# Optimization experiments

Hardware: AMD Instinct MI355X
Metric: run time of the kernel (lower is better)

The kernel has to match this reference:

```python
import jax, jax.numpy as jnp
import numpy as np

B, C, V = 4096, 1000, 8000   # batch, NUM_COMPO, NUM_CHARS
THRESH = 0.8                 # compo_score_thresh
SCALE = 0.1                  # score_adjustment_scale
TOPK = 5


def setup_inputs() -> dict:
    key = jax.random.key(0)
    k1, k2, k3, k4 = jax.random.split(key, 4)
    return {
        "pred_class_logits": jax.random.normal(k1, (B, V), jnp.float32),
        "pred_compo_logits": jax.random.normal(k2, (B, C), jnp.float32),
        "compo_co_occurrence_prob": jax.random.uniform(k3, (C, C), dtype=jnp.float32),
        "compo_chinese_matrix": jax.random.randint(k4, (C, V), 0, 2, dtype=jnp.int32),
    }


def _decode_one(compo_scores, co_occ, matrix):
    """components_to_chinese_char for one sample. compo_scores:[C], co_occ:[C,C], matrix:[C,V]."""
    nC, nV = matrix.shape
    # score adjustment from co-occurrence of components above threshold
    sel = compo_scores > THRESH                                   # [C]
    adj = SCALE * jnp.sum(
        jnp.where(sel[:, None], co_occ * compo_scores[:, None], 0.0), axis=0)  # [C]
    scores = compo_scores + adj
    max_idx = jnp.argmax(scores)
    max_score = scores[max_idx]
    # re-threshold and sort selected scores descending (fixed-shape: mask with -inf)
    sel2 = scores > THRESH
    num_selected = jnp.sum(sel2.astype(jnp.int32))
    masked = jnp.where(sel2, scores, -jnp.inf)
    order = jnp.argsort(-masked)          # descending; selected compo indices first
    sorted_scores = masked[order]
    hit0 = matrix[max_idx]                # [V] 0/1

    def cond(carry):
        i, hit, _ = carry
        return (i < num_selected) & (jnp.sum(hit) > 1)

    def body(carry):
        i, hit, _ = carry
        row = matrix[order[i]]
        new_hit = jnp.where(hit + row == 2, 1, 0).astype(jnp.int32)  # intersection
        return (i + 1, new_hit, hit)

    i0 = jnp.array(1, jnp.int32)
    i, hit, prev = jax.lax.while_loop(cond, body, (i0, hit0, hit0))
    empty = jnp.sum(hit) == 0
    i = jnp.where(empty, i - 1, i)
    hit = jnp.where(empty, prev, hit)
    hit_score = jnp.where(i == 1, max_score, sorted_scores[jnp.maximum(i - 1, 0)])
    # first 5 hit char indices (ascending, as tf.where yields), padded with -1
    char_ids = jnp.where(hit == 1, jnp.arange(nV), nV)
    first5 = jnp.sort(char_ids)[:TOPK]
    hit_indices = jnp.where(first5 == nV, -1, first5).astype(jnp.int32)
    return hit_indices, hit_score


def reference(pred_class_logits, pred_compo_logits, compo_co_occurrence_prob, compo_chinese_matrix):
    class_probs = jax.nn.softmax(pred_class_logits, axis=1)            # [B,V]
    class_scores, class_indices = jax.lax.top_k(class_probs, TOPK)     # [B,5]
    compo_scores = jax.nn.sigmoid(pred_compo_logits)                   # [B,C]
    hit_indices, hit_scores = jax.vmap(_decode_one, in_axes=(0, None, None))(
        compo_scores, compo_co_occurrence_prob, compo_chinese_matrix)
    class_indices = class_indices.astype(jnp.int32)
    num_hit = jnp.sum((hit_indices != -1).astype(jnp.int32), axis=1)   # [B]
    combined1 = jnp.where(num_hit == 1, hit_indices[:, 0], class_indices[:, 0])
    combined2 = jnp.where((class_scores[:, 0] < 0.85) & (num_hit == 1),
                          hit_indices[:, 0], class_indices[:, 0])
    return (class_indices, class_scores, hit_indices, hit_scores, combined1, combined2)
```

## Files before the change

### kernel.cpp

```cpp
#include <hip/hip_runtime.h>
#include <cstdint>
#include <cstddef>

typedef unsigned long long u64;

#define B_SZ 4096
#define C_SZ 1000
#define V_SZ 8000
#define RW 128
#define THRESHF 0.8f
#define SCALEF 0.1f

#define OFF_CI 0
#define OFF_CS (B_SZ * 5)
#define OFF_HI (2 * B_SZ * 5)
#define OFF_HS (3 * B_SZ * 5)
#define OFF_C1 (3 * B_SZ * 5 + B_SZ)
#define OFF_C2 (3 * B_SZ * 5 + 2 * B_SZ)

__global__ __launch_bounds__(256) void pack_kernel(const int* __restrict__ mat,
                                                   u64* __restrict__ packed) {
  const int c = blockIdx.x;
  const int tid = threadIdx.x;
  const int lane = tid & 63;
  const int wv = tid >> 6;
  const int* row = mat + (size_t)c * V_SZ;
  for (int base = 0; base < 8192; base += 256) {
    const int k = base + tid;
    int v = 0;
    if (k < V_SZ) v = row[k];
    u64 msk = __ballot(v != 0);
    if (lane == 0) packed[(size_t)c * RW + ((base >> 6) + wv)] = msk;
  }
}

__global__ __launch_bounds__(256) void class_topk_kernel(const float* __restrict__ logits,
                                                         float* __restrict__ out) {
  const int b = blockIdx.x;
  const int tid = threadIdx.x;
  const int lane = tid & 63;
  const int wv = tid >> 6;
  const float* row = logits + (size_t)b * V_SZ;
  float v[32];
#pragma unroll
  for (int f = 0; f < 8; ++f) {
    const int base = (f << 10) + (tid << 2);
    if (base < V_SZ) {
      float4 x = *(const float4*)(row + base);
      v[4 * f + 0] = x.x; v[4 * f + 1] = x.y; v[4 * f + 2] = x.z; v[4 * f + 3] = x.w;
    } else {
      v[4 * f + 0] = -INFINITY; v[4 * f + 1] = -INFINITY;
      v[4 * f + 2] = -INFINITY; v[4 * f + 3] = -INFINITY;
    }
  }
  __shared__ float sred[4];
  __shared__ int sredi[4];
  float lm = -INFINITY;
#pragma unroll
  for (int q = 0; q < 32; ++q) lm = fmaxf(lm, v[q]);
#pragma unroll
  for (int o = 32; o >= 1; o >>= 1) lm = fmaxf(lm, __shfl_xor(lm, o));
  if (lane == 0) sred[wv] = lm;
  __syncthreads();
  const float m = fmaxf(fmaxf(sred[0], sred[1]), fmaxf(sred[2], sred[3]));
  float ls = 0.f;
#pragma unroll
  for (int q = 0; q < 32; ++q) ls += expf(v[q] - m);
#pragma unroll
  for (int o = 32; o >= 1; o >>= 1) ls += __shfl_xor(ls, o);
  __syncthreads();
  if (lane == 0) sred[wv] = ls;
  __syncthreads();
  const float ssum = sred[0] + sred[1] + sred[2] + sred[3];
  for (int r = 0; r < 5; ++r) {
    float bv = -INFINITY;
    int bi = 0;
#pragma unroll
    for (int q = 0; q < 32; ++q) {
      const int idx = ((q >> 2) << 10) + (tid << 2) + (q & 3);
      if (v[q] > bv) { bv = v[q]; bi = idx; }
    }
#pragma unroll
    for (int o = 32; o >= 1; o >>= 1) {
      float ov = __shfl_xor(bv, o);
      int oi = __shfl_xor(bi, o);
      if (ov > bv || (ov == bv && oi < bi)) { bv = ov; bi = oi; }
    }
    __syncthreads();
    if (lane == 0) { sred[wv] = bv; sredi[wv] = bi; }
    __syncthreads();
    bv = sred[0]; bi = sredi[0];
#pragma unroll
    for (int w = 1; w < 4; ++w) {
      if (sred[w] > bv || (sred[w] == bv && sredi[w] < bi)) { bv = sred[w]; bi = sredi[w]; }
    }
    if (((bi & 1023) >> 2) == tid) {
      const int sl = ((bi >> 10) << 2) | (bi & 3);
#pragma unroll
      for (int q = 0; q < 32; ++q)
        if (q == sl) v[q] = -INFINITY;
    }
    if (tid == 0) {
      out[OFF_CI + b * 5 + r] = (float)bi;
      out[OFF_CS + b * 5 + r] = expf(bv - m) / ssum;
    }
  }
}

__global__ __launch_bounds__(256, 4) void decode_kernel(const float* __restrict__ compo_logits,
                                                        const float* __restrict__ co_occ,
                                                        const u64* __restrict__ packed,
                                                        float* __restrict__ out) {
  const int tid = threadIdx.x;
  const int lane = tid & 63;
  const int w = tid >> 6;
  const int b = blockIdx.x * 4 + w;
  __shared__ short s_idx[4][512];
  __shared__ float s_val[4][512];

  const float4* lg4 = (const float4*)(compo_logits + (size_t)b * C_SZ);
  float raw[16];
#pragma unroll
  for (int p = 0; p < 4; ++p) {
    const int fi = lane + (p << 6);
    if (fi < 250) {
      float4 x = lg4[fi];
      raw[4 * p + 0] = 1.0f / (1.0f + expf(-x.x));
      raw[4 * p + 1] = 1.0f / (1.0f + expf(-x.y));
      raw[4 * p + 2] = 1.0f / (1.0f + expf(-x.z));
      raw[4 * p + 3] = 1.0f / (1.0f + expf(-x.w));
    } else {
      raw[4 * p + 0] = 0.f; raw[4 * p + 1] = 0.f; raw[4 * p + 2] = 0.f; raw[4 * p + 3] = 0.f;
    }
  }
  int n = 0;
#pragma unroll
  for (int p = 0; p < 4; ++p) {
    unsigned mb = 0;
    if (raw[4 * p + 0] > THRESHF) mb |= 1u;
    if (raw[4 * p + 1] > THRESHF) mb |= 2u;
    if (raw[4 * p + 2] > THRESHF) mb |= 4u;
    if (raw[4 * p + 3] > THRESHF) mb |= 8u;
    const int cnt = __popc(mb);
    int inc = cnt;
#pragma unroll
    for (int o = 1; o < 64; o <<= 1) {
      int t = __shfl_up(inc, o);
      if (lane >= o) inc += t;
    }
    int off = n + inc - cnt;
    const int total = __shfl(inc, 63);
#pragma unroll
    for (int j = 0; j < 4; ++j) {
      if (mb & (1u << j)) {
        s_idx[w][off] = (short)((p << 8) + (lane << 2) + j);
        s_val[w][off] = raw[4 * p + j];
        ++off;
      }
    }
    n += total;
  }
  if (lane < 4) { s_idx[w][n + lane] = 0; s_val[w][n + lane] = 0.0f; }

  float4 acc0 = {0, 0, 0, 0}, acc1 = {0, 0, 0, 0}, acc2 = {0, 0, 0, 0}, acc3 = {0, 0, 0, 0};
  {
    const float4* cop = (const float4*)co_occ;
    const int l0 = lane, l1 = lane + 64, l2 = lane + 128, l3 = lane + 192;
    const bool g3 = lane < 58;
    for (int e = 0; e < n; e += 4) {
      const int i0 = s_idx[w][e + 0]; const float m0 = s_val[w][e + 0];
      const int i1 = s_idx[w][e + 1]; const float m1 = s_val[w][e + 1];
      const int i2 = s_idx[w][e + 2]; const float m2 = s_val[w][e + 2];
      const int i3 = s_idx[w][e + 3]; const float m3 = s_val[w][e + 3];
      const float4* r0 = cop + (size_t)i0 * 250;
      const float4* r1 = cop + (size_t)i1 * 250;
      const float4* r2 = cop + (size_t)i2 * 250;
      const float4* r3 = cop + (size_t)i3 * 250;
      float4 a0 = r0[l0], a1 = r0[l1], a2 = r0[l2];
      float4 b0 = r1[l0], b1 = r1[l1], b2 = r1[l2];
      float4 d0 = r2[l0], d1 = r2[l1], d2 = r2[l2];
      float4 e0 = r3[l0], e1 = r3[l1], e2 = r3[l2];
      float4 a3 = {0, 0, 0, 0}, b3 = {0, 0, 0, 0}, d3 = {0, 0, 0, 0}, e3 = {0, 0, 0, 0};
      if (g3) { a3 = r0[l3]; b3 = r1[l3]; d3 = r2[l3]; e3 = r3[l3]; }
      acc0.x += m0 * a0.x; acc0.y += m0 * a0.y; acc0.z += m0 * a0.z; acc0.w += m0 * a0.w;
      acc1.x += m0 * a1.x; acc1.y += m0 * a1.y; acc1.z += m0 * a1.z; acc1.w += m0 * a1.w;
      acc2.x += m0 * a2.x; acc2.y += m0 * a2.y; acc2.z += m0 * a2.z; acc2.w += m0 * a2.w;
      acc3.x += m0 * a3.x; acc3.y += m0 * a3.y; acc3.z += m0 * a3.z; acc3.w += m0 * a3.w;
      acc0.x += m1 * b0.x; acc0.y += m1 * b0.y; acc0.z += m1 * b0.z; acc0.w += m1 * b0.w;
      acc1.x += m1 * b1.x; acc1.y += m1 * b1.y; acc1.z += m1 * b1.z; acc1.w += m1 * b1.w;
      acc2.x += m1 * b2.x; acc2.y += m1 * b2.y; acc2.z += m1 * b2.z; acc2.w += m1 * b2.w;
      acc3.x += m1 * b3.x; acc3.y += m1 * b3.y; acc3.z += m1 * b3.z; acc3.w += m1 * b3.w;
      acc0.x += m2 * d0.x; acc0.y += m2 * d0.y; acc0.z += m2 * d0.z; acc0.w += m2 * d0.w;
      acc1.x += m2 * d1.x; acc1.y += m2 * d1.y; acc1.z += m2 * d1.z; acc1.w += m2 * d1.w;
      acc2.x += m2 * d2.x; acc2.y += m2 * d2.y; acc2.z += m2 * d2.z; acc2.w += m2 * d2.w;
      acc3.x += m2 * d3.x; acc3.y += m2 * d3.y; acc3.z += m2 * d3.z; acc3.w += m2 * d3.w;
      acc0.x += m3 * e0.x; acc0.y += m3 * e0.y; acc0.z += m3 * e0.z; acc0.w += m3 * e0.w;
      acc1.x += m3 * e1.x; acc1.y += m3 * e1.y; acc1.z += m3 * e1.z; acc1.w += m3 * e1.w;
      acc2.x += m3 * e2.x; acc2.y += m3 * e2.y; acc2.z += m3 * e2.z; acc2.w += m3 * e2.w;
      acc3.x += m3 * e3.x; acc3.y += m3 * e3.y; acc3.z += m3 * e3.z; acc3.w += m3 * e3.w;
    }
  }
  float fin[16];
  fin[0] = raw[0] + SCALEF * acc0.x;  fin[1] = raw[1] + SCALEF * acc0.y;
  fin[2] = raw[2] + SCALEF * acc0.z;  fin[3] = raw[3] + SCALEF * acc0.w;
  fin[4] = raw[4] + SCALEF * acc1.x;  fin[5] = raw[5] + SCALEF * acc1.y;
  fin[6] = raw[6] + SCALEF * acc1.z;  fin[7] = raw[7] + SCALEF * acc1.w;
  fin[8] = raw[8] + SCALEF * acc2.x;  fin[9] = raw[9] + SCALEF * acc2.y;
  fin[10] = raw[10] + SCALEF * acc2.z; fin[11] = raw[11] + SCALEF * acc2.w;
  fin[12] = raw[12] + SCALEF * acc3.x; fin[13] = raw[13] + SCALEF * acc3.y;
  fin[14] = raw[14] + SCALEF * acc3.z; fin[15] = raw[15] + SCALEF * acc3.w;

  u64 key[16];
  unsigned avail = 0;
  int cnt = 0;
  u64 kb = 0;
#pragma unroll
  for (int q = 0; q < 16; ++q) {
    const int col = (lane << 2) + (q & 3) + ((q >> 2) << 8);
    if (col < C_SZ) {
      const float f = fin[q];
      const u64 k = ((u64)__float_as_uint(f) << 32) | (u64)(0xFFFFFFFFu - (unsigned)col);
      key[q] = k;
      if (k > kb) kb = k;
      if (f > THRESHF) { avail |= 1u << q; cnt++; }
    } else key[q] = 0;
  }
  u64 mk = kb;
#pragma unroll
  for (int o = 32; o >= 1; o >>= 1) { u64 t = __shfl_xor(mk, o); if (t > mk) mk = t; }
  const float mxv = __uint_as_float((unsigned)(mk >> 32));
  const int mxi = (int)(0xFFFFFFFFu - (unsigned)(mk & 0xFFFFFFFFull));
#pragma unroll
  for (int o = 32; o >= 1; o >>= 1) cnt += __shfl_xor(cnt, o);
  const int nsel = cnt;
  if (((mxi >> 2) & 63) == lane) avail &= ~(1u << ((mxi & 3) | ((mxi >> 8) << 2)));
  const u64* pr = packed + (size_t)mxi * RW;
  u64 h0 = pr[lane], h1 = pr[64 + lane];
  int pc = __popcll(h0) + __popcll(h1);
#pragma unroll
  for (int o = 32; o >= 1; o >>= 1) pc += __shfl_xor(pc, o);
  int ii = 1;
  float last_val = mxv;
  if (nsel >= 2 && pc > 1) {
    for (;;) {
      int kt = (nsel - ii < 8) ? (nsel - ii) : 8;
      float cval[8];
      int cidx[8];
      u64 rl[8], rh[8];
      float lastc = last_val;
      int kv = 0;
#pragma unroll
      for (int k = 0; k < 8; ++k) {
        cval[k] = 0.0f; cidx[k] = -1;
        if (k < kt) {
          u64 lm = 0;
#pragma unroll
          for (int q = 0; q < 16; ++q)
            if (avail & (1u << q)) { if (key[q] > lm) lm = key[q]; }
          u64 ck = lm;
#pragma unroll
          for (int o = 32; o >= 1; o >>= 1) { u64 t = __shfl_xor(ck, o); if (t > ck) ck = t; }
          if (ck != 0) {
            cval[k] = __uint_as_float((unsigned)(ck >> 32));
            cidx[k] = (int)(0xFFFFFFFFu - (unsigned)(ck & 0xFFFFFFFFull));
            if (((cidx[k] >> 2) & 63) == lane)
              avail &= ~(1u << ((cidx[k] & 3) | ((cidx[k] >> 8) << 2)));
            lastc = cval[k];
            kv = k + 1;
          }
        }
      }
      kt = kv;
      if (kt == 0) break;
#pragma unroll
      for (int k = 0; k < 8; ++k) {
        if (k < kt) {
          const u64* rp2 = packed + (size_t)cidx[k] * RW;
          rl[k] = rp2[lane]; rh[k] = rp2[64 + lane];
        } else { rl[k] = ~0ull; rh[k] = ~0ull; }
      }
      u64 c0 = h0, c1 = h1, pk0 = 0, pk1 = 0;
#pragma unroll
      for (int k = 0; k < 8; ++k) {
        c0 &= rl[k]; c1 &= rh[k];
        const u64 p = (u64)(__popcll(c0) + __popcll(c1));
        if (k < 4) pk0 |= p << (k * 16); else pk1 |= p << ((k - 4) * 16);
      }
#pragma unroll
      for (int o = 32; o >= 1; o >>= 1) { pk0 += __shfl_xor(pk0, o); pk1 += __shfl_xor(pk1, o); }
      int kstar = -1;
      unsigned pcv = 0;
#pragma unroll
      for (int k = 0; k < 8; ++k) {
        if (k < kt && kstar < 0) {
          const unsigned f = (unsigned)(((k < 4 ? pk0 : pk1) >> ((k & 3) * 16)) & 0xFFFFull);
          if (f <= 1u) { kstar = k; pcv = f; }
        }
      }
      if (kstar >= 0) {
        float vk = 0.f, vkm1 = last_val;
#pragma unroll
        for (int k = 0; k < 8; ++k)
          if (k == kstar) { vk = cval[k]; if (k > 0) vkm1 = cval[k - 1]; }
        const int na = (pcv == 1u) ? (kstar + 1) : kstar;
#pragma unroll
        for (int k = 0; k < 8; ++k) if (k < na) { h0 &= rl[k]; h1 &= rh[k]; }
        if (pcv == 1u) { ii += kstar + 1; last_val = vk; }
        else { ii += kstar; last_val = vkm1; }
        break;
      }
#pragma unroll
      for (int k = 0; k < 8; ++k) if (k < kt) { h0 &= rl[k]; h1 &= rh[k]; }
      ii += kt;
      last_val = lastc;
      if (ii >= nsel) break;
    }
  }
  const float hit_score = (ii == 1) ? mxv : last_val;

  const int c0n = __popcll(h0), c1n = __popcll(h1);
  int s0 = c0n;
#pragma unroll
  for (int o = 1; o < 64; o <<= 1) {
    int nn = __shfl_up(s0, o);
    if (lane >= o) s0 += nn;
  }
  const int tot0 = __shfl(s0, 63);
  const int pre0 = s0 - c0n;
  int s1 = c1n;
#pragma unroll
  for (int o = 1; o < 64; o <<= 1) {
    int nn = __shfl_up(s1, o);
    if (lane >= o) s1 += nn;
  }
  const int tot = tot0 + __shfl(s1, 63);
  const int pre1 = tot0 + s1 - c1n;
  {
    u64 x = h0;
    int r = pre0;
    while (x && r < 5) {
      const int bp = __ffsll((unsigned long long)x) - 1;
      out[OFF_HI + b * 5 + r] = (float)((lane << 6) + bp);
      x &= x - 1;
      ++r;
    }
    x = h1;
    r = pre1;
    while (x && r < 5) {
      const int bp = __ffsll((unsigned long long)x) - 1;
      out[OFF_HI + b * 5 + r] = (float)(((64 + lane) << 6) + bp);
      x &= x - 1;
      ++r;
    }
  }
  int fb = 0x7fffffff;
  if (c0n) fb = (lane << 6) + __ffsll((unsigned long long)h0) - 1;
  else if (c1n) fb = ((64 + lane) << 6) + __ffsll((unsigned long long)h1) - 1;
#pragma unroll
  for (int o = 32; o >= 1; o >>= 1) fb = min(fb, __shfl_xor(fb, o));
  if (lane == 0) {
    const int num_hit = tot < 5 ? tot : 5;
    for (int r = num_hit; r < 5; ++r) out[OFF_HI + b * 5 + r] = -1.0f;
    out[OFF_HS + b] = hit_score;
    const float ci0 = out[OFF_CI + b * 5];
    const float cs0 = out[OFF_CS + b * 5];
    out[OFF_C1 + b] = (num_hit == 1) ? (float)fb : ci0;
    out[OFF_C2 + b] = (cs0 < 0.85f && num_hit == 1) ? (float)fb : ci0;
  }
}

extern "C" void kernel_launch(void* const* d_in, const int* in_sizes, int n_in,
                              void* d_out, int out_size, void* d_ws, size_t ws_size,
                              hipStream_t stream) {
  (void)in_sizes; (void)n_in; (void)out_size; (void)ws_size;
  const float* class_logits = (const float*)d_in[0];
  const float* compo_logits = (const float*)d_in[1];
  const float* co_occ = (const float*)d_in[2];
  const int* mat = (const int*)d_in[3];
  float* out = (float*)d_out;
  u64* packed = (u64*)d_ws;

  pack_kernel<<<C_SZ, 256, 0, stream>>>(mat, packed);
  class_topk_kernel<<<B_SZ, 256, 0, stream>>>(class_logits, out);
  decode_kernel<<<B_SZ / 4, 256, 0, stream>>>(compo_logits, co_occ, packed, out);
}
```

Measured before the change: 133.5 us.

## Merge class top-k and decode into one heterogeneous kernel with epilogue

```diff
diff --git a/kernel.cpp b/kernel.cpp
--- a/kernel.cpp
+++ b/kernel.cpp
@@ -34,87 +34,92 @@
   }
 }
 
-__global__ __launch_bounds__(256) void class_topk_kernel(const float* __restrict__ logits,
-                                                         float* __restrict__ out) {
-  const int b = blockIdx.x;
+__global__ __launch_bounds__(256, 4) void main_kernel(const float* __restrict__ class_logits,
+                                                      const float* __restrict__ compo_logits,
+                                                      const float* __restrict__ co_occ,
+                                                      const u64* __restrict__ packed,
+                                                      float* __restrict__ out,
+                                                      int* __restrict__ ws_nh,
+                                                      int* __restrict__ ws_fb) {
+  const int bid = blockIdx.x;
+  const int g = bid / 5;
+  const int r5 = bid - g * 5;
   const int tid = threadIdx.x;
   const int lane = tid & 63;
   const int wv = tid >> 6;
-  const float* row = logits + (size_t)b * V_SZ;
-  float v[32];
-#pragma unroll
-  for (int f = 0; f < 8; ++f) {
-    const int base = (f << 10) + (tid << 2);
-    if (base < V_SZ) {
-      float4 x = *(const float4*)(row + base);
-      v[4 * f + 0] = x.x; v[4 * f + 1] = x.y; v[4 * f + 2] = x.z; v[4 * f + 3] = x.w;
-    } else {
-      v[4 * f + 0] = -INFINITY; v[4 * f + 1] = -INFINITY;
-      v[4 * f + 2] = -INFINITY; v[4 * f + 3] = -INFINITY;
-    }
-  }
-  __shared__ float sred[4];
-  __shared__ int sredi[4];
-  float lm = -INFINITY;
-#pragma unroll
-  for (int q = 0; q < 32; ++q) lm = fmaxf(lm, v[q]);
-#pragma unroll
-  for (int o = 32; o >= 1; o >>= 1) lm = fmaxf(lm, __shfl_xor(lm, o));
-  if (lane == 0) sred[wv] = lm;
-  __syncthreads();
-  const float m = fmaxf(fmaxf(sred[0], sred[1]), fmaxf(sred[2], sred[3]));
-  float ls = 0.f;
-#pragma unroll
-  for (int q = 0; q < 32; ++q) ls += expf(v[q] - m);
-#pragma unroll
-  for (int o = 32; o >= 1; o >>= 1) ls += __shfl_xor(ls, o);
-  __syncthreads();
-  if (lane == 0) sred[wv] = ls;
-  __syncthreads();
-  const float ssum = sred[0] + sred[1] + sred[2] + sred[3];
-  for (int r = 0; r < 5; ++r) {
-    float bv = -INFINITY;
-    int bi = 0;
-#pragma unroll
-    for (int q = 0; q < 32; ++q) {
-      const int idx = ((q >> 2) << 10) + (tid << 2) + (q & 3);
-      if (v[q] > bv) { bv = v[q]; bi = idx; }
-    }
-#pragma unroll
-    for (int o = 32; o >= 1; o >>= 1) {
-      float ov = __shfl_xor(bv, o);
-      int oi = __shfl_xor(bi, o);
-      if (ov > bv || (ov == bv && oi < bi)) { bv = ov; bi = oi; }
-    }
+
+  if (r5 != 0) {
+    const int b = g * 4 + (r5 - 1);
+    const float* row = class_logits + (size_t)b * V_SZ;
+    float v[32];
+#pragma unroll
+    for (int f = 0; f < 8; ++f) {
+      const int base = (f << 10) + (tid << 2);
+      if (base < V_SZ) {
+        float4 x = *(const float4*)(row + base);
+        v[4 * f + 0] = x.x; v[4 * f + 1] = x.y; v[4 * f + 2] = x.z; v[4 * f + 3] = x.w;
+      } else {
+        v[4 * f + 0] = -INFINITY; v[4 * f + 1] = -INFINITY;
+        v[4 * f + 2] = -INFINITY; v[4 * f + 3] = -INFINITY;
+      }
+    }
+    __shared__ float sred[4];
+    __shared__ int sredi[4];
+    float lm = -INFINITY;
+#pragma unroll
+    for (int q = 0; q < 32; ++q) lm = fmaxf(lm, v[q]);
+#pragma unroll
+    for (int o = 32; o >= 1; o >>= 1) lm = fmaxf(lm, __shfl_xor(lm, o));
+    if (lane == 0) sred[wv] = lm;
     __syncthreads();
-    if (lane == 0) { sred[wv] = bv; sredi[wv] = bi; }
+    const float m = fmaxf(fmaxf(sred[0], sred[1]), fmaxf(sred[2], sred[3]));
+    float ls = 0.f;
+#pragma unroll
+    for (int q = 0; q < 32; ++q) ls += expf(v[q] - m);
+#pragma unroll
+    for (int o = 32; o >= 1; o >>= 1) ls += __shfl_xor(ls, o);
     __syncthreads();
-    bv = sred[0]; bi = sredi[0];
-#pragma unroll
-    for (int w = 1; w < 4; ++w) {
-      if (sred[w] > bv || (sred[w] == bv && sredi[w] < bi)) { bv = sred[w]; bi = sredi[w]; }
-    }
-    if (((bi & 1023) >> 2) == tid) {
-      const int sl = ((bi >> 10) << 2) | (bi & 3);
-#pragma unroll
-      for (int q = 0; q < 32; ++q)
-        if (q == sl) v[q] = -INFINITY;
-    }
-    if (tid == 0) {
-      out[OFF_CI + b * 5 + r] = (float)bi;
-      out[OFF_CS + b * 5 + r] = expf(bv - m) / ssum;
-    }
-  }
-}
-
-__global__ __launch_bounds__(256, 4) void decode_kernel(const float* __restrict__ compo_logits,
-                                                        const float* __restrict__ co_occ,
-                                                        const u64* __restrict__ packed,
-                                                        float* __restrict__ out) {
-  const int tid = threadIdx.x;
-  const int lane = tid & 63;
-  const int w = tid >> 6;
-  const int b = blockIdx.x * 4 + w;
+    if (lane == 0) sred[wv] = ls;
+    __syncthreads();
+    const float ssum = sred[0] + sred[1] + sred[2] + sred[3];
+    for (int rr = 0; rr < 5; ++rr) {
+      float bv = -INFINITY;
+      int bi = 0;
+#pragma unroll
+      for (int q = 0; q < 32; ++q) {
+        const int idx = ((q >> 2) << 10) + (tid << 2) + (q & 3);
+        if (v[q] > bv) { bv = v[q]; bi = idx; }
+      }
+#pragma unroll
+      for (int o = 32; o >= 1; o >>= 1) {
+        float ov = __shfl_xor(bv, o);
+        int oi = __shfl_xor(bi, o);
+        if (ov > bv || (ov == bv && oi < bi)) { bv = ov; bi = oi; }
+      }
+      __syncthreads();
+      if (lane == 0) { sred[wv] = bv; sredi[wv] = bi; }
+      __syncthreads();
+      bv = sred[0]; bi = sredi[0];
+#pragma unroll
+      for (int w2 = 1; w2 < 4; ++w2) {
+        if (sred[w2] > bv || (sred[w2] == bv && sredi[w2] < bi)) { bv = sred[w2]; bi = sredi[w2]; }
+      }
+      if (((bi & 1023) >> 2) == tid) {
+        const int sl = ((bi >> 10) << 2) | (bi & 3);
+#pragma unroll
+        for (int q = 0; q < 32; ++q)
+          if (q == sl) v[q] = -INFINITY;
+      }
+      if (tid == 0) {
+        out[OFF_CI + b * 5 + rr] = (float)bi;
+        out[OFF_CS + b * 5 + rr] = expf(bv - m) / ssum;
+      }
+    }
+    return;
+  }
+
+  const int w = wv;
+  const int b = g * 4 + w;
   __shared__ short s_idx[4][512];
   __shared__ float s_val[4][512];
 
@@ -141,14 +146,14 @@
     if (raw[4 * p + 1] > THRESHF) mb |= 2u;
     if (raw[4 * p + 2] > THRESHF) mb |= 4u;
     if (raw[4 * p + 3] > THRESHF) mb |= 8u;
-    const int cnt = __popc(mb);
-    int inc = cnt;
+    const int cnt4 = __popc(mb);
+    int inc = cnt4;
 #pragma unroll
     for (int o = 1; o < 64; o <<= 1) {
       int t = __shfl_up(inc, o);
       if (lane >= o) inc += t;
     }
-    int off = n + inc - cnt;
+    int off = n + inc - cnt4;
     const int total = __shfl(inc, 63);
 #pragma unroll
     for (int j = 0; j < 4; ++j) {
@@ -253,11 +258,11 @@
       for (int k = 0; k < 8; ++k) {
         cval[k] = 0.0f; cidx[k] = -1;
         if (k < kt) {
-          u64 lm = 0;
+          u64 lm2 = 0;
 #pragma unroll
           for (int q = 0; q < 16; ++q)
-            if (avail & (1u << q)) { if (key[q] > lm) lm = key[q]; }
-          u64 ck = lm;
+            if (avail & (1u << q)) { if (key[q] > lm2) lm2 = key[q]; }
+          u64 ck = lm2;
 #pragma unroll
           for (int o = 32; o >= 1; o >>= 1) { u64 t = __shfl_xor(ck, o); if (t > ck) ck = t; }
           if (ck != 0) {
@@ -337,20 +342,20 @@
   const int pre1 = tot0 + s1 - c1n;
   {
     u64 x = h0;
-    int r = pre0;
-    while (x && r < 5) {
+    int rr = pre0;
+    while (x && rr < 5) {
       const int bp = __ffsll((unsigned long long)x) - 1;
-      out[OFF_HI + b * 5 + r] = (float)((lane << 6) + bp);
+      out[OFF_HI + b * 5 + rr] = (float)((lane << 6) + bp);
       x &= x - 1;
-      ++r;
+      ++rr;
     }
     x = h1;
-    r = pre1;
-    while (x && r < 5) {
+    rr = pre1;
+    while (x && rr < 5) {
       const int bp = __ffsll((unsigned long long)x) - 1;
-      out[OFF_HI + b * 5 + r] = (float)(((64 + lane) << 6) + bp);
+      out[OFF_HI + b * 5 + rr] = (float)(((64 + lane) << 6) + bp);
       x &= x - 1;
-      ++r;
+      ++rr;
     }
   }
   int fb = 0x7fffffff;
@@ -360,12 +365,24 @@
   for (int o = 32; o >= 1; o >>= 1) fb = min(fb, __shfl_xor(fb, o));
   if (lane == 0) {
     const int num_hit = tot < 5 ? tot : 5;
-    for (int r = num_hit; r < 5; ++r) out[OFF_HI + b * 5 + r] = -1.0f;
+    for (int rr = num_hit; rr < 5; ++rr) out[OFF_HI + b * 5 + rr] = -1.0f;
     out[OFF_HS + b] = hit_score;
+    ws_nh[b] = num_hit;
+    ws_fb[b] = fb;
+  }
+}
+
+__global__ __launch_bounds__(256) void epilogue_kernel(const int* __restrict__ ws_nh,
+                                                       const int* __restrict__ ws_fb,
+                                                       float* __restrict__ out) {
+  const int b = blockIdx.x * 256 + threadIdx.x;
+  if (b < B_SZ) {
     const float ci0 = out[OFF_CI + b * 5];
     const float cs0 = out[OFF_CS + b * 5];
-    out[OFF_C1 + b] = (num_hit == 1) ? (float)fb : ci0;
-    out[OFF_C2 + b] = (cs0 < 0.85f && num_hit == 1) ? (float)fb : ci0;
+    const int nh = ws_nh[b];
+    const float fbv = (float)ws_fb[b];
+    out[OFF_C1 + b] = (nh == 1) ? fbv : ci0;
+    out[OFF_C2 + b] = (cs0 < 0.85f && nh == 1) ? fbv : ci0;
   }
 }
 
@@ -379,8 +396,11 @@
   const int* mat = (const int*)d_in[3];
   float* out = (float*)d_out;
   u64* packed = (u64*)d_ws;
+  int* ws_nh = (int*)((char*)d_ws + (size_t)C_SZ * RW * 8);
+  int* ws_fb = ws_nh + B_SZ;
 
   pack_kernel<<<C_SZ, 256, 0, stream>>>(mat, packed);
-  class_topk_kernel<<<B_SZ, 256, 0, stream>>>(class_logits, out);
-  decode_kernel<<<B_SZ / 4, 256, 0, stream>>>(compo_logits, co_occ, packed, out);
+  main_kernel<<<5 * (B_SZ / 4), 256, 0, stream>>>(class_logits, compo_logits, co_occ,
+                                                  packed, out, ws_nh, ws_fb);
+  epilogue_kernel<<<(B_SZ + 255) / 256, 256, 0, stream>>>(ws_nh, ws_fb, out);
 }
```

New measurement: 152.3 us. 1.14x slower.
